# Optimization experiments

Measured on AMD Instinct MI355X. Metric: run time of the kernel, lower is better.

The kernel has to match this reference:

```python
import jax, jax.numpy as jnp
import numpy as np

B, S, D = 2, 2048, 2048
NH, NKV = 16, 4
HD = D // NH          # 128
Q_DIM = NH * HD       # 2048
KV_DIM = NKV * HD     # 512
N_REP = NH // NKV     # 4


def setup_inputs() -> dict:
    key = jax.random.key(0)
    k1, k2, k3, k4 = jax.random.split(key, 4)
    x = jax.random.normal(k1, (B, S, D), dtype=jnp.float32)
    freqs_cis = jax.random.normal(k2, (S, HD), dtype=jnp.float32)
    Wqkv = jax.random.normal(k3, (Q_DIM + 2 * KV_DIM, D), dtype=jnp.float32) * (D ** -0.5)
    Wo = jax.random.normal(k4, (D, Q_DIM), dtype=jnp.float32) * (Q_DIM ** -0.5)
    return {"x": x, "freqs_cis": freqs_cis, "Wqkv": Wqkv, "Wo": Wo}


def _apply_rope(xq, xk, freqs_cis):
    # xq: [B,S,NH,HD], xk: [B,S,NKV,HD], freqs_cis: [S,HD] viewed as [S,1,HD//2,2]
    f = freqs_cis.reshape(S, 1, HD // 2, 2)
    f0, f1 = f[..., 0], f[..., 1]  # broadcast over batch & heads

    def rot(t):
        shp = t.shape
        tp = t.reshape(*shp[:-1], HD // 2, 2)
        t0, t1 = tp[..., 0], tp[..., 1]
        # row1 = <x, (f0,f1)>;  row0 = <x, (f1,-f0)>  (matches torch flip+negate)
        row1 = t0 * f0 + t1 * f1
        row0 = t0 * f1 - t1 * f0
        return jnp.stack([row0, row1], axis=-1).reshape(shp)

    return rot(xq), rot(xk)


def reference(x, freqs_cis, Wqkv, Wo):
    # Fused QKV projection (exact path: all RLA sketch dims = 0)
    xqkv = jnp.einsum('bsd,od->bso', x, Wqkv)
    xq = xqkv[..., :Q_DIM].reshape(B, S, NH, HD)
    xk = xqkv[..., Q_DIM:Q_DIM + KV_DIM].reshape(B, S, NKV, HD)
    xv = xqkv[..., Q_DIM + KV_DIM:].reshape(B, S, NKV, HD)

    xq, xk = _apply_rope(xq, xk, freqs_cis)

    # [B,H,S,HD]
    xq = xq.transpose(0, 2, 1, 3)
    xk = xk.transpose(0, 2, 1, 3)
    xv = xv.transpose(0, 2, 1, 3)

    # GQA: repeat kv heads n_rep times
    xk = jnp.repeat(xk, N_REP, axis=1)
    xv = jnp.repeat(xv, N_REP, axis=1)

    scale = 1.0 / jnp.sqrt(jnp.asarray(HD, dtype=xq.dtype))
    scores = jnp.einsum('bhqd,bhkd->bhqk', xq, xk) * scale
    causal = jnp.tril(jnp.ones((S, S), dtype=bool))
    scores = jnp.where(causal, scores, jnp.finfo(scores.dtype).min)
    probs = jax.nn.softmax(scores, axis=-1)
    out = jnp.einsum('bhqk,bhkd->bhqd', probs, xv)  # [B,H,S,HD]

    out = out.transpose(0, 2, 1, 3).reshape(B, S, Q_DIM)
    return jnp.einsum('bsq,dq->bsd', out, Wo)
```

## Files before the change

kernel.cpp:

```cpp
#include <hip/hip_runtime.h>
#include <hip/hip_bf16.h>
#include <cstdint>
#include <cstddef>

#define B_ 2
#define S_ 2048
#define NH_ 16
#define NKV_ 4
#define HD_ 128
#define QDIM_ 2048
#define KVDIM_ 512
#define QKV_ 3072

typedef __attribute__((ext_vector_type(8))) short short8;
typedef __attribute__((ext_vector_type(4))) float float4v;

__device__ __forceinline__ float bf2f(short u) {
  union { unsigned int i; float f; } v;
  v.i = ((unsigned int)(unsigned short)u) << 16;
  return v.f;
}
__device__ __forceinline__ short f2bf(float f) {
  union { float f; unsigned int i; } v; v.f = f;
  unsigned int x = v.i;
  x += 0x7fffu + ((x >> 16) & 1u);
  return (short)(x >> 16);
}

__device__ __forceinline__ void async_copy16(void* lds, const void* g) {
  __builtin_amdgcn_global_load_lds(
      (const __attribute__((address_space(1))) void*)g,
      (__attribute__((address_space(3))) void*)lds, 16, 0, 0);
}

__global__ void f32_to_bf16(const float* __restrict__ src, short* __restrict__ dst,
                            int n8) {
  int id = blockIdx.x * 256 + threadIdx.x;
  if (id >= n8) return;
  const float* f = src + (size_t)id * 8;
  float4v a = *(const float4v*)(f);
  float4v b = *(const float4v*)(f + 4);
  short8 r;
#pragma unroll
  for (int e = 0; e < 4; ++e) { r[e] = f2bf(a[e]); r[4 + e] = f2bf(b[e]); }
  *(short8*)(dst + (size_t)id * 8) = r;
}

template <int N, int K, bool CF32>
__global__ __launch_bounds__(256)
void gemm_nt_bf16(const short* __restrict__ A, const short* __restrict__ Bm,
                  void* __restrict__ Cp) {
  __shared__ __align__(16) short sA[128 * 32];
  __shared__ __align__(16) short sB[128 * 32];
  const int tid = threadIdx.x;
  const int m0 = blockIdx.y * 128, n0 = blockIdx.x * 128;
  const int wave = tid >> 6, lane = tid & 63;
  const int wm = (wave & 1) << 6, wn = (wave >> 1) << 6;
  const int lm = lane & 15, kg = lane >> 4;

  float4v acc[4][4];
#pragma unroll
  for (int i = 0; i < 4; ++i)
#pragma unroll
    for (int j = 0; j < 4; ++j)
      acc[i][j] = (float4v){0.f, 0.f, 0.f, 0.f};

  const int r0 = tid >> 2, c0 = tid & 3;
  const short* gA0 = A + (size_t)(m0 + r0) * K + c0 * 8;
  const short* gA1 = gA0 + (size_t)64 * K;
  const short* gB0 = Bm + (size_t)(n0 + r0) * K + c0 * 8;
  const short* gB1 = gB0 + (size_t)64 * K;
  short* lA0 = sA + tid * 8;
  short* lA1 = sA + 2048 + tid * 8;
  short* lB0 = sB + tid * 8;
  short* lB1 = sB + 2048 + tid * 8;

  for (int k0 = 0; k0 < K; k0 += 32) {
    async_copy16(lA0, gA0 + k0);
    async_copy16(lA1, gA1 + k0);
    async_copy16(lB0, gB0 + k0);
    async_copy16(lB1, gB1 + k0);
    __syncthreads();

    short8 a[4], b[4];
#pragma unroll
    for (int i = 0; i < 4; ++i)
      a[i] = *(const short8*)(sA + (wm + i * 16 + lm) * 32 + kg * 8);
#pragma unroll
    for (int j = 0; j < 4; ++j)
      b[j] = *(const short8*)(sB + (wn + j * 16 + lm) * 32 + kg * 8);
#pragma unroll
    for (int i = 0; i < 4; ++i)
#pragma unroll
      for (int j = 0; j < 4; ++j)
        acc[i][j] = __builtin_amdgcn_mfma_f32_16x16x32_bf16(a[i], b[j], acc[i][j], 0, 0, 0);
    __syncthreads();
  }

#pragma unroll
  for (int i = 0; i < 4; ++i) {
    const int rb = m0 + wm + i * 16 + kg * 4;
#pragma unroll
    for (int j = 0; j < 4; ++j) {
      const int cc = n0 + wn + j * 16 + lm;
#pragma unroll
      for (int r = 0; r < 4; ++r) {
        if constexpr (CF32)
          ((float*)Cp)[(size_t)(rb + r) * N + cc] = acc[i][j][r];
        else
          ((short*)Cp)[(size_t)(rb + r) * N + cc] = f2bf(acc[i][j][r]);
      }
    }
  }
}

__global__ void rope_split(const short* __restrict__ xqkv, const float* __restrict__ freqs,
                           short* __restrict__ Qr, short* __restrict__ Kr,
                           short* __restrict__ Vv) {
  const int id = blockIdx.x * 256 + threadIdx.x;
  const int i = id / (QKV_ / 8);
  const int c8 = id % (QKV_ / 8);
  const int col = c8 * 8;
  const int b = i >> 11, s = i & (S_ - 1);
  short8 xv = *(const short8*)(xqkv + (size_t)i * QKV_ + col);
  if (col < QDIM_ + KVDIM_) {
    int d;
    short* dst;
    float sc;
    if (col < QDIM_) {
      int hh = col >> 7; d = col & 127;
      dst = Qr + ((size_t)(b * NH_ + hh) * S_ + s) * HD_ + d;
      sc = 0.08838834764831845f;
    } else {
      int cc = col - QDIM_;
      int hh = cc >> 7; d = cc & 127;
      dst = Kr + ((size_t)(b * NKV_ + hh) * S_ + s) * HD_ + d;
      sc = 1.0f;
    }
    const float* fp = freqs + (size_t)s * HD_ + d;
    float4v fa = *(const float4v*)(fp);
    float4v fb = *(const float4v*)(fp + 4);
    float ff[8] = {fa[0], fa[1], fa[2], fa[3], fb[0], fb[1], fb[2], fb[3]};
    short8 ov;
#pragma unroll
    for (int pp = 0; pp < 4; ++pp) {
      float t0 = bf2f(xv[2 * pp]), t1 = bf2f(xv[2 * pp + 1]);
      float f0 = ff[2 * pp], f1 = ff[2 * pp + 1];
      ov[2 * pp]     = f2bf((t0 * f1 - t1 * f0) * sc);
      ov[2 * pp + 1] = f2bf((t0 * f0 + t1 * f1) * sc);
    }
    *(short8*)dst = ov;
  } else {
    int cc = col - QDIM_ - KVDIM_;
    int hh = cc >> 7, d = cc & 127;
    *(short8*)(Vv + ((size_t)(b * NKV_ + hh) * S_ + s) * HD_ + d) = xv;
  }
}

__global__ void transpose_v(const short* __restrict__ Vv, short* __restrict__ Vt) {
  __shared__ short t[64][72];
  const int s0 = blockIdx.x * 64, d0 = blockIdx.y * 64;
  const short* src = Vv + (size_t)blockIdx.z * S_ * HD_;
  short* dst = Vt + (size_t)blockIdx.z * S_ * HD_;
  const int tid = threadIdx.x;
#pragma unroll
  for (int c = 0; c < 2; ++c) {
    int ch = tid + 256 * c;
    int row = ch >> 3, kc = ch & 7;
    *(short8*)(&t[row][kc * 8]) =
        *(const short8*)(src + (size_t)(s0 + row) * HD_ + d0 + kc * 8);
  }
  __syncthreads();
#pragma unroll
  for (int c = 0; c < 2; ++c) {
    int ch = tid + 256 * c;
    int drow = ch >> 3, sc = ch & 7;
    short8 w;
#pragma unroll
    for (int j = 0; j < 8; ++j) w[j] = t[sc * 8 + j][drow];
    *(short8*)(dst + (size_t)(d0 + drow) * S_ + s0 + sc * 8) = w;
  }
}

#define TK 64
#define VP 72

__global__ __launch_bounds__(256)
void attn_causal(const short* __restrict__ Q, const short* __restrict__ K,
                 const short* __restrict__ Vt, short* __restrict__ O) {
  const int pair = blockIdx.x;
  const int bh = blockIdx.y;
  const int b = bh >> 4, h = bh & 15;
  const int kvh = h >> 2;
  const int tid = threadIdx.x, wave = tid >> 6, lane = tid & 63;
  const int lm = lane & 15, kg = lane >> 4;

  __shared__ __align__(16) short sK[TK * HD_];
  __shared__ __align__(16) short sVt[HD_ * TK];
  __shared__ __align__(16) short sP[64 * VP];

  const short* Qb = Q + (size_t)(b * NH_ + h) * S_ * HD_;
  const short* Kb = K + (size_t)(b * NKV_ + kvh) * S_ * HD_;
  const short* Vtb = Vt + (size_t)(b * NKV_ + kvh) * S_ * HD_;

  const int krow0 = tid >> 4, kkc0 = tid & 15;
  const int vrow0 = tid >> 3, vkc0 = tid & 7;

  for (int half = 0; half < 2; ++half) {
    const int qt = (half == 0) ? pair : 31 - pair;
    const int q0w = qt * 64 + wave * 16;

    short8 qf[4];
#pragma unroll
    for (int kk = 0; kk < 4; ++kk)
      qf[kk] = *(const short8*)(Qb + (size_t)(q0w + lm) * HD_ + kk * 32 + kg * 8);

    float mrow[4], lrow[4];
    float4v o[8];
#pragma unroll
    for (int r = 0; r < 4; ++r) { mrow[r] = -1e9f; lrow[r] = 0.f; }
#pragma unroll
    for (int df = 0; df < 8; ++df) o[df] = (float4v){0.f, 0.f, 0.f, 0.f};

    const int ntiles = qt + 1;
    for (int j = 0; j < ntiles; ++j) {
      const int k0 = j * TK;
#pragma unroll
      for (int c = 0; c < 4; ++c) {
        int ch = tid + 256 * c;
        int row = (c & 1) ? (krow0 + 16 * (c >> 0)) : krow0;
        (void)row;
      }
#pragma unroll
      for (int c = 0; c < 4; ++c) {
        int ch = tid + 256 * c;
        int row = ch >> 4, kc = ch & 15;
        async_copy16(sK + ch * 8,
                     Kb + (size_t)(k0 + row) * HD_ + (kc ^ (row & 7)) * 8);
      }
#pragma unroll
      for (int c = 0; c < 4; ++c) {
        int ch = tid + 256 * c;
        int row = ch >> 3, kc = ch & 7;
        async_copy16(sVt + ch * 8,
                     Vtb + (size_t)row * S_ + k0 + (kc ^ (row & 7)) * 8);
      }
      __syncthreads();

      float4v sf[4];
#pragma unroll
      for (int nj = 0; nj < 4; ++nj) sf[nj] = (float4v){0.f, 0.f, 0.f, 0.f};
#pragma unroll
      for (int kk = 0; kk < 4; ++kk) {
        int kd = kk * 4 + kg;
#pragma unroll
        for (int nj = 0; nj < 4; ++nj) {
          int n = nj * 16 + lm;
          short8 bf = *(const short8*)(sK + n * HD_ + (kd ^ (n & 7)) * 8);
          sf[nj] = __builtin_amdgcn_mfma_f32_16x16x32_bf16(qf[kk], bf, sf[nj], 0, 0, 0);
        }
      }

      const bool diag = (j == qt);
#pragma unroll
      for (int r = 0; r < 4; ++r) {
        float pv[4];
        float mx = -3e38f;
        if (diag) {
          const int qloc = wave * 16 + kg * 4 + r;
#pragma unroll
          for (int nj = 0; nj < 4; ++nj) {
            float v = ((nj * 16 + lm) <= qloc) ? sf[nj][r] : -3e38f;
            pv[nj] = v; mx = fmaxf(mx, v);
          }
        } else {
#pragma unroll
          for (int nj = 0; nj < 4; ++nj) {
            float v = sf[nj][r];
            pv[nj] = v; mx = fmaxf(mx, v);
          }
        }
        mx = fmaxf(mx, __shfl_xor(mx, 1, 64));
        mx = fmaxf(mx, __shfl_xor(mx, 2, 64));
        mx = fmaxf(mx, __shfl_xor(mx, 4, 64));
        mx = fmaxf(mx, __shfl_xor(mx, 8, 64));
        float mold = mrow[r];
        float mnew = fmaxf(mold, mx);
        float alpha = __expf(fminf(mold - mnew, 0.f));
        float rs = 0.f;
#pragma unroll
        for (int nj = 0; nj < 4; ++nj) {
          float e = __expf(fminf(pv[nj] - mnew, 0.f));
          rs += e;
          sP[(wave * 16 + kg * 4 + r) * VP + nj * 16 + lm] = f2bf(e);
        }
        rs += __shfl_xor(rs, 1, 64);
        rs += __shfl_xor(rs, 2, 64);
        rs += __shfl_xor(rs, 4, 64);
        rs += __shfl_xor(rs, 8, 64);
        mrow[r] = mnew;
        lrow[r] = lrow[r] * alpha + rs;
#pragma unroll
        for (int df = 0; df < 8; ++df) o[df][r] *= alpha;
      }

#pragma unroll
      for (int kst = 0; kst < 2; ++kst) {
        short8 pa = *(const short8*)(sP + (wave * 16 + lm) * VP + kst * 32 + kg * 8);
        int kd = kst * 4 + kg;
#pragma unroll
        for (int df = 0; df < 8; ++df) {
          int n = df * 16 + lm;
          short8 vf = *(const short8*)(sVt + n * TK + (kd ^ (n & 7)) * 8);
          o[df] = __builtin_amdgcn_mfma_f32_16x16x32_bf16(pa, vf, o[df], 0, 0, 0);
        }
      }
      __syncthreads();
    }

#pragma unroll
    for (int r = 0; r < 4; ++r) {
      float inv = 1.f / lrow[r];
      const size_t rowoff =
          (size_t)(b * S_ + q0w + kg * 4 + r) * QDIM_ + h * HD_;
#pragma unroll
      for (int df = 0; df < 8; ++df)
        O[rowoff + df * 16 + lm] = f2bf(o[df][r] * inv);
    }
  }
}

extern "C" void kernel_launch(void* const* d_in, const int* in_sizes, int n_in,
                              void* d_out, int out_size, void* d_ws, size_t ws_size,
                              hipStream_t stream) {
  const float* x     = (const float*)d_in[0];
  const float* freqs = (const float*)d_in[1];
  const float* Wqkv  = (const float*)d_in[2];
  const float* Wo    = (const float*)d_in[3];
  float* out = (float*)d_out;

  short* ws     = (short*)d_ws;
  short* xb     = ws;
  short* Wob    = ws;
  short* Wqkvb  = ws + (size_t)4096 * 2048;
  short* xqkv   = Wqkvb + (size_t)QKV_ * 2048;
  short* attn   = xqkv;
  short* Qr     = xqkv + (size_t)4096 * QKV_;
  short* Kr     = Qr + (size_t)B_ * NH_ * S_ * HD_;
  short* Vv     = Kr + (size_t)B_ * NKV_ * S_ * HD_;
  short* Vtg    = Vv + (size_t)B_ * NKV_ * S_ * HD_;

  f32_to_bf16<<<(4096 * 2048 / 8) / 256, 256, 0, stream>>>(x, xb, 4096 * 2048 / 8);
  f32_to_bf16<<<(QKV_ * 2048 / 8) / 256, 256, 0, stream>>>(Wqkv, Wqkvb, QKV_ * 2048 / 8);
  gemm_nt_bf16<QKV_, 2048, false>
      <<<dim3(QKV_ / 128, 4096 / 128), 256, 0, stream>>>(xb, Wqkvb, xqkv);
  f32_to_bf16<<<(2048 * 2048 / 8) / 256, 256, 0, stream>>>(Wo, Wob, 2048 * 2048 / 8);
  rope_split<<<(B_ * S_ * QKV_ / 8) / 256, 256, 0, stream>>>(xqkv, freqs, Qr, Kr, Vv);
  transpose_v<<<dim3(S_ / 64, HD_ / 64, B_ * NKV_), 256, 0, stream>>>(Vv, Vtg);
  attn_causal<<<dim3(16, B_ * NH_), 256, 0, stream>>>(Qr, Kr, Vtg, attn);
  gemm_nt_bf16<2048, 2048, true>
      <<<dim3(2048 / 128, 4096 / 128), 256, 0, stream>>>(attn, Wob, out);
}
```

Before: 337.6 us.

## Compute transposed attention scores to keep P in registers, skipping LDS round-trip

The attention kernel now computes S^T = K·Q^T, so each lane holds a column of scores for one query row. The softmax reduction then needs only two cross-lane shuffles, and the bf16 probabilities feed the PV MFMA (16x16x16) straight from registers instead of passing through an LDS buffer. The output epilogue is staged through per-wave LDS so each lane writes 16-byte vectors to global memory. The trade-off is twice as many, smaller PV MFMA instructions and narrower 8-byte V loads from LDS.

```diff
diff --git a/kernel.cpp b/kernel.cpp
--- a/kernel.cpp
+++ b/kernel.cpp
@@ -13,6 +13,7 @@
 #define QKV_ 3072
 
 typedef __attribute__((ext_vector_type(8))) short short8;
+typedef __attribute__((ext_vector_type(4))) short bhalf4;
 typedef __attribute__((ext_vector_type(4))) float float4v;
 
 __device__ __forceinline__ float bf2f(short u) {
@@ -183,7 +184,6 @@
 }
 
 #define TK 64
-#define VP 72
 
 __global__ __launch_bounds__(256)
 void attn_causal(const short* __restrict__ Q, const short* __restrict__ K,
@@ -197,40 +197,30 @@
 
   __shared__ __align__(16) short sK[TK * HD_];
   __shared__ __align__(16) short sVt[HD_ * TK];
-  __shared__ __align__(16) short sP[64 * VP];
+  __shared__ __align__(16) short sO[4 * 16 * 128];
 
   const short* Qb = Q + (size_t)(b * NH_ + h) * S_ * HD_;
   const short* Kb = K + (size_t)(b * NKV_ + kvh) * S_ * HD_;
   const short* Vtb = Vt + (size_t)(b * NKV_ + kvh) * S_ * HD_;
 
-  const int krow0 = tid >> 4, kkc0 = tid & 15;
-  const int vrow0 = tid >> 3, vkc0 = tid & 7;
-
   for (int half = 0; half < 2; ++half) {
     const int qt = (half == 0) ? pair : 31 - pair;
     const int q0w = qt * 64 + wave * 16;
+    const int qglob = q0w + lm;
 
     short8 qf[4];
 #pragma unroll
     for (int kk = 0; kk < 4; ++kk)
-      qf[kk] = *(const short8*)(Qb + (size_t)(q0w + lm) * HD_ + kk * 32 + kg * 8);
-
-    float mrow[4], lrow[4];
+      qf[kk] = *(const short8*)(Qb + (size_t)qglob * HD_ + kk * 32 + kg * 8);
+
+    float mcur = -1e9f, lcur = 0.f;
     float4v o[8];
-#pragma unroll
-    for (int r = 0; r < 4; ++r) { mrow[r] = -1e9f; lrow[r] = 0.f; }
 #pragma unroll
     for (int df = 0; df < 8; ++df) o[df] = (float4v){0.f, 0.f, 0.f, 0.f};
 
     const int ntiles = qt + 1;
     for (int j = 0; j < ntiles; ++j) {
       const int k0 = j * TK;
-#pragma unroll
-      for (int c = 0; c < 4; ++c) {
-        int ch = tid + 256 * c;
-        int row = (c & 1) ? (krow0 + 16 * (c >> 0)) : krow0;
-        (void)row;
-      }
 #pragma unroll
       for (int c = 0; c < 4; ++c) {
         int ch = tid + 256 * c;
@@ -247,85 +237,90 @@
       }
       __syncthreads();
 
-      float4v sf[4];
-#pragma unroll
-      for (int nj = 0; nj < 4; ++nj) sf[nj] = (float4v){0.f, 0.f, 0.f, 0.f};
+      float4v sfT[4];
+#pragma unroll
+      for (int mj = 0; mj < 4; ++mj) sfT[mj] = (float4v){0.f, 0.f, 0.f, 0.f};
 #pragma unroll
       for (int kk = 0; kk < 4; ++kk) {
         int kd = kk * 4 + kg;
 #pragma unroll
-        for (int nj = 0; nj < 4; ++nj) {
-          int n = nj * 16 + lm;
-          short8 bf = *(const short8*)(sK + n * HD_ + (kd ^ (n & 7)) * 8);
-          sf[nj] = __builtin_amdgcn_mfma_f32_16x16x32_bf16(qf[kk], bf, sf[nj], 0, 0, 0);
+        for (int mj = 0; mj < 4; ++mj) {
+          int row = mj * 16 + lm;
+          short8 af = *(const short8*)(sK + row * HD_ + (kd ^ (row & 7)) * 8);
+          sfT[mj] = __builtin_amdgcn_mfma_f32_16x16x32_bf16(af, qf[kk], sfT[mj], 0, 0, 0);
         }
       }
 
-      const bool diag = (j == qt);
-#pragma unroll
-      for (int r = 0; r < 4; ++r) {
-        float pv[4];
-        float mx = -3e38f;
-        if (diag) {
-          const int qloc = wave * 16 + kg * 4 + r;
-#pragma unroll
-          for (int nj = 0; nj < 4; ++nj) {
-            float v = ((nj * 16 + lm) <= qloc) ? sf[nj][r] : -3e38f;
-            pv[nj] = v; mx = fmaxf(mx, v);
+      if (j == qt) {
+#pragma unroll
+        for (int mj = 0; mj < 4; ++mj)
+#pragma unroll
+          for (int r = 0; r < 4; ++r) {
+            int kcol = k0 + mj * 16 + kg * 4 + r;
+            sfT[mj][r] = (kcol <= qglob) ? sfT[mj][r] : -3e38f;
           }
-        } else {
-#pragma unroll
-          for (int nj = 0; nj < 4; ++nj) {
-            float v = sf[nj][r];
-            pv[nj] = v; mx = fmaxf(mx, v);
-          }
+      }
+
+      float mx = -3e38f;
+#pragma unroll
+      for (int mj = 0; mj < 4; ++mj)
+#pragma unroll
+        for (int r = 0; r < 4; ++r) mx = fmaxf(mx, sfT[mj][r]);
+      mx = fmaxf(mx, __shfl_xor(mx, 16, 64));
+      mx = fmaxf(mx, __shfl_xor(mx, 32, 64));
+      float mnew = fmaxf(mcur, mx);
+      float alpha = __expf(fminf(mcur - mnew, 0.f));
+      float rs = 0.f;
+      bhalf4 pb[4];
+#pragma unroll
+      for (int t = 0; t < 4; ++t)
+#pragma unroll
+        for (int r = 0; r < 4; ++r) {
+          float e = __expf(fminf(sfT[t][r] - mnew, 0.f));
+          rs += e;
+          pb[t][r] = f2bf(e);
         }
-        mx = fmaxf(mx, __shfl_xor(mx, 1, 64));
-        mx = fmaxf(mx, __shfl_xor(mx, 2, 64));
-        mx = fmaxf(mx, __shfl_xor(mx, 4, 64));
-        mx = fmaxf(mx, __shfl_xor(mx, 8, 64));
-        float mold = mrow[r];
-        float mnew = fmaxf(mold, mx);
-        float alpha = __expf(fminf(mold - mnew, 0.f));
-        float rs = 0.f;
-#pragma unroll
-        for (int nj = 0; nj < 4; ++nj) {
-          float e = __expf(fminf(pv[nj] - mnew, 0.f));
-          rs += e;
-          sP[(wave * 16 + kg * 4 + r) * VP + nj * 16 + lm] = f2bf(e);
+      rs += __shfl_xor(rs, 16, 64);
+      rs += __shfl_xor(rs, 32, 64);
+      mcur = mnew;
+      lcur = lcur * alpha + rs;
+#pragma unroll
+      for (int df = 0; df < 8; ++df)
+#pragma unroll
+        for (int r = 0; r < 4; ++r) o[df][r] *= alpha;
+
+#pragma unroll
+      for (int t = 0; t < 4; ++t) {
+        int kc = t * 2 + (kg >> 1);
+#pragma unroll
+        for (int df = 0; df < 8; ++df) {
+          int row = df * 16 + lm;
+          bhalf4 va = *(const bhalf4*)(sVt + row * TK + (kc ^ (row & 7)) * 8 +
+                                       (kg & 1) * 4);
+          o[df] = __builtin_amdgcn_mfma_f32_16x16x16bf16_1k(va, pb[t], o[df], 0, 0, 0);
         }
-        rs += __shfl_xor(rs, 1, 64);
-        rs += __shfl_xor(rs, 2, 64);
-        rs += __shfl_xor(rs, 4, 64);
-        rs += __shfl_xor(rs, 8, 64);
-        mrow[r] = mnew;
-        lrow[r] = lrow[r] * alpha + rs;
-#pragma unroll
-        for (int df = 0; df < 8; ++df) o[df][r] *= alpha;
-      }
-
-#pragma unroll
-      for (int kst = 0; kst < 2; ++kst) {
-        short8 pa = *(const short8*)(sP + (wave * 16 + lm) * VP + kst * 32 + kg * 8);
-        int kd = kst * 4 + kg;
-#pragma unroll
-        for (int df = 0; df < 8; ++df) {
-          int n = df * 16 + lm;
-          short8 vf = *(const short8*)(sVt + n * TK + (kd ^ (n & 7)) * 8);
-          o[df] = __builtin_amdgcn_mfma_f32_16x16x32_bf16(pa, vf, o[df], 0, 0, 0);
-        }
       }
       __syncthreads();
     }
 
-#pragma unroll
-    for (int r = 0; r < 4; ++r) {
-      float inv = 1.f / lrow[r];
-      const size_t rowoff =
-          (size_t)(b * S_ + q0w + kg * 4 + r) * QDIM_ + h * HD_;
-#pragma unroll
-      for (int df = 0; df < 8; ++df)
-        O[rowoff + df * 16 + lm] = f2bf(o[df][r] * inv);
+    float inv = 1.f / lcur;
+    short* myO = sO + wave * 2048;
+#pragma unroll
+    for (int df = 0; df < 8; ++df) {
+      unsigned int p0 = (unsigned short)f2bf(o[df][0] * inv) |
+                        ((unsigned int)(unsigned short)f2bf(o[df][1] * inv) << 16);
+      unsigned int p1 = (unsigned short)f2bf(o[df][2] * inv) |
+                        ((unsigned int)(unsigned short)f2bf(o[df][3] * inv) << 16);
+      int base = lm * 128 + df * 16 + kg * 4;
+      *(unsigned int*)(myO + base) = p0;
+      *(unsigned int*)(myO + base + 2) = p1;
+    }
+    int q = lane >> 2, dp = (lane & 3) * 32;
+    const size_t rowoff = (size_t)(b * S_ + q0w + q) * QDIM_ + h * HD_ + dp;
+#pragma unroll
+    for (int e = 0; e < 4; ++e) {
+      short8 w = *(const short8*)(myO + q * 128 + dp + e * 8);
+      *(short8*)(O + rowoff + e * 8) = w;
     }
   }
 }
```

Result: faster. 328.7 us (-2.6%).
